# Kernel optimization log

Hardware: AMD Instinct MI355X
Metric: run time of the kernel (lower is better)

The kernel has to match this reference:

```python
import jax, jax.numpy as jnp
import numpy as np

B, S, D = 4, 4096, 1024
STATE = 1024
HID = 4 * D
EPS_NORM = 1e-6           # RMSNorm module eps
EPS_FP32 = 1.1920929e-7   # torch F.rms_norm default eps = finfo(fp32).eps


def rms_norm(x, eps):
    # no learned weight (RMSNorm(dim=-1) has weight=None)
    return x * jax.lax.rsqrt(jnp.mean(jnp.square(x), axis=-1, keepdims=True) + eps)


def setup_inputs() -> dict:
    key = jax.random.key(0)
    ks = jax.random.split(key, 8)
    scale_d = 1.0 / np.sqrt(D)
    scale_s = 1.0 / np.sqrt(STATE)
    scale_h = 1.0 / np.sqrt(HID)
    return {
        "x": jax.random.normal(ks[0], (B, S, D), jnp.float32),
        "x0": jax.random.normal(ks[1], (B, S, D), jnp.float32),
        "Wu": jax.random.normal(ks[2], (STATE, D), jnp.float32) * scale_d,
        "Wg": jax.random.normal(ks[3], (STATE, D), jnp.float32) * scale_d,
        "Wo": jax.random.normal(ks[4], (D, STATE), jnp.float32) * scale_s,
        "Wfc": jax.random.normal(ks[5], (HID, D), jnp.float32) * scale_d,
        "Wproj": jax.random.normal(ks[6], (D, HID), jnp.float32) * scale_h,
        "memory_mix": jnp.ones((D,), jnp.float32),
        "mlp_scale": jnp.ones((D,), jnp.float32),
        "resid_mix": jnp.stack([jnp.ones((D,), jnp.float32), jnp.zeros((D,), jnp.float32)]),
    }


def reference(x, x0, Wu, Wg, Wo, Wfc, Wproj, memory_mix, mlp_scale, resid_mix):
    # residual mix of x and x0
    x = resid_mix[0][None, None, :] * x + resid_mix[1][None, None, :] * x0

    # --- CausalPrefixMemory branch ---
    h = rms_norm(x, EPS_NORM)
    update = jnp.einsum('bsd,kd->bsk', h, Wu)
    gate = jax.nn.sigmoid(jnp.einsum('bsd,kd->bsk', h, Wg))
    memory = jnp.cumsum(gate * update, axis=1)          # [B,S,STATE]
    denom = jnp.arange(1, S + 1, dtype=jnp.float32)[None, :, None]
    m = rms_norm(memory / denom, EPS_FP32)
    mem_out = jnp.einsum('bsk,dk->bsd', m, Wo)
    x = x + memory_mix[None, None, :] * mem_out

    # --- MLP branch: relu^2 ---
    h2 = rms_norm(x, EPS_NORM)
    r = jax.nn.relu(jnp.einsum('bsd,hd->bsh', h2, Wfc))
    mlp_out = jnp.einsum('bsh,dh->bsd', jnp.square(r), Wproj)
    x = x + mlp_scale[None, None, :] * mlp_out
    return x
```

## Files before the change

kernel.cpp:

```cpp
#include <hip/hip_runtime.h>
#include <stdint.h>

typedef unsigned short u16;
typedef __attribute__((ext_vector_type(8))) short s16x8;
typedef __attribute__((ext_vector_type(4))) float f32x4;

__device__ __forceinline__ u16 f2bf(float f) {
  uint32_t u = __float_as_uint(f);
  uint32_t r = (u + 0x7FFFu + ((u >> 16) & 1u)) >> 16;
  return (u16)r;
}

__device__ __forceinline__ void gll16(const void* g, void* lds) {
  __builtin_amdgcn_global_load_lds(
      (const __attribute__((address_space(1))) uint32_t*)g,
      (__attribute__((address_space(3))) uint32_t*)lds, 16, 0, 0);
}

__device__ __forceinline__ void xcd_swz(int& bx, int& by) {
  int gx = gridDim.x;
  int lin = blockIdx.y * gx + blockIdx.x;
  int cpx = (gx * gridDim.y) >> 3;
  int nl = (lin & 7) * cpx + (lin >> 3);
  bx = nl % gx;
  by = nl / gx;
}

__global__ __launch_bounds__(256) void k_f2b(const float* __restrict__ src,
                                             u16* __restrict__ dst, int n) {
  int i = (blockIdx.x * 256 + threadIdx.x) * 4;
  if (i < n) {
    float4 v = *(const float4*)(src + i);
    ushort4 o;
    o.x = f2bf(v.x); o.y = f2bf(v.y); o.z = f2bf(v.z); o.w = f2bf(v.w);
    *(ushort4*)(dst + i) = o;
  }
}

template <bool MIX>
__global__ __launch_bounds__(256) void k_rms(const float* __restrict__ X,
                                             const float* __restrict__ X0,
                                             const float* __restrict__ rmix,
                                             float* __restrict__ XMout,
                                             u16* __restrict__ Hout, float eps) {
  const int row = blockIdx.x, t = threadIdx.x;
  const size_t base = (size_t)row * 1024;
  float4 v;
  if (MIX) {
    float4 a = ((const float4*)(X + base))[t];
    float4 b = ((const float4*)(X0 + base))[t];
    float4 c0 = ((const float4*)rmix)[t];
    float4 c1 = ((const float4*)(rmix + 1024))[t];
    v.x = c0.x * a.x + c1.x * b.x;
    v.y = c0.y * a.y + c1.y * b.y;
    v.z = c0.z * a.z + c1.z * b.z;
    v.w = c0.w * a.w + c1.w * b.w;
  } else {
    v = ((const float4*)(X + base))[t];
  }
  float ss = v.x * v.x + v.y * v.y + v.z * v.z + v.w * v.w;
#pragma unroll
  for (int o = 32; o > 0; o >>= 1) ss += __shfl_xor(ss, o);
  __shared__ float red[4];
  if ((t & 63) == 0) red[t >> 6] = ss;
  __syncthreads();
  float tot = red[0] + red[1] + red[2] + red[3];
  float sc = rsqrtf(tot * (1.0f / 1024.0f) + eps);
  if (MIX) ((float4*)(XMout + base))[t] = v;
  ushort4 hv;
  hv.x = f2bf(v.x * sc); hv.y = f2bf(v.y * sc);
  hv.z = f2bf(v.z * sc); hv.w = f2bf(v.w * sc);
  ((ushort4*)(Hout + base))[t] = hv;
}

__global__ __launch_bounds__(256) void k_rms_mem(const float* __restrict__ Mem,
                                                 u16* __restrict__ Mout) {
  const int row = blockIdx.x, t = threadIdx.x;
  const float inv = 1.0f / (float)((row & 4095) + 1);
  const size_t base = (size_t)row * 1024;
  float4 v = ((const float4*)(Mem + base))[t];
  v.x *= inv; v.y *= inv; v.z *= inv; v.w *= inv;
  float ss = v.x * v.x + v.y * v.y + v.z * v.z + v.w * v.w;
#pragma unroll
  for (int o = 32; o > 0; o >>= 1) ss += __shfl_xor(ss, o);
  __shared__ float red[4];
  if ((t & 63) == 0) red[t >> 6] = ss;
  __syncthreads();
  float tot = red[0] + red[1] + red[2] + red[3];
  float sc = rsqrtf(tot * (1.0f / 1024.0f) + 1.1920929e-7f);
  ushort4 hv;
  hv.x = f2bf(v.x * sc); hv.y = f2bf(v.y * sc);
  hv.z = f2bf(v.z * sc); hv.w = f2bf(v.w * sc);
  ((ushort4*)(Mout + base))[t] = hv;
}

__global__ __launch_bounds__(256) void k_scan1(const float* __restrict__ P,
                                               float* __restrict__ CS) {
  int blk = blockIdx.x;
  int kt = blk & 3, chunk = (blk >> 2) & 15, b = blk >> 6;
  int k = kt * 256 + threadIdx.x;
  const float* p = P + ((size_t)b * 4096 + (size_t)chunk * 256) * 1024 + k;
  float s = 0.f;
#pragma unroll 8
  for (int i = 0; i < 256; ++i) s += p[(size_t)i * 1024];
  CS[((size_t)b * 16 + chunk) * 1024 + k] = s;
}

__global__ __launch_bounds__(256) void k_scan2(float* __restrict__ CS) {
  int idx = blockIdx.x * 256 + threadIdx.x;
  int b = idx >> 10, k = idx & 1023;
  float run = 0.f;
  for (int c = 0; c < 16; ++c) {
    size_t o = ((size_t)b * 16 + c) * 1024 + k;
    float v = CS[o];
    CS[o] = run;
    run += v;
  }
}

__global__ __launch_bounds__(256) void k_scan3(float* __restrict__ P,
                                               const float* __restrict__ CS) {
  int blk = blockIdx.x;
  int kt = blk & 3, chunk = (blk >> 2) & 15, b = blk >> 6;
  int k = kt * 256 + threadIdx.x;
  float run = CS[((size_t)b * 16 + chunk) * 1024 + k];
  float* p = P + ((size_t)b * 4096 + (size_t)chunk * 256) * 1024 + k;
#pragma unroll 8
  for (int i = 0; i < 256; ++i) {
    run += p[(size_t)i * 1024];
    p[(size_t)i * 1024] = run;
  }
}

__global__ __launch_bounds__(256, 2) void gemm_dual(
    const u16* __restrict__ A, const u16* __restrict__ Bu,
    const u16* __restrict__ Bg, float* __restrict__ P, int K) {
  __shared__ __align__(16) u16 As[128 * 64];
  __shared__ __align__(16) u16 Us[64 * 64];
  __shared__ __align__(16) u16 Gs[64 * 64];
  const int t = threadIdx.x;
  const int lane = t & 63, wid = t >> 6;
  int bx, by;
  xcd_swz(bx, by);
  const int m0 = by * 128, n0 = bx * 64;
  const int wm = wid * 32;
  const int l15 = lane & 15, lhi = lane >> 4;

  size_t gA[4], gU[2];
#pragma unroll
  for (int i = 0; i < 4; ++i) {
    int j = i * 256 + t;
    int row = j >> 3;
    int k16 = (j & 7) ^ (row & 7);
    gA[i] = (size_t)(m0 + row) * K + k16 * 8;
  }
#pragma unroll
  for (int i = 0; i < 2; ++i) {
    int j = i * 256 + t;
    int row = j >> 3;
    int k16 = (j & 7) ^ (row & 7);
    gU[i] = (size_t)(n0 + row) * K + k16 * 8;
  }

  f32x4 au[2][4], ag[2][4];
#pragma unroll
  for (int mi = 0; mi < 2; ++mi)
#pragma unroll
    for (int ni = 0; ni < 4; ++ni) { au[mi][ni] = 0.0f; ag[mi][ni] = 0.0f; }

  for (int kb = 0; kb < K; kb += 64) {
#pragma unroll
    for (int i = 0; i < 4; ++i) {
      int j = i * 256 + t;
      gll16(A + gA[i] + kb, &As[j * 8]);
    }
#pragma unroll
    for (int i = 0; i < 2; ++i) {
      int j = i * 256 + t;
      gll16(Bu + gU[i] + kb, &Us[j * 8]);
      gll16(Bg + gU[i] + kb, &Gs[j * 8]);
    }
    __syncthreads();
#pragma unroll
    for (int kc = 0; kc < 2; ++kc) {
      s16x8 af[2], uf[4], gf[4];
#pragma unroll
      for (int mi = 0; mi < 2; ++mi) {
        int row = wm + mi * 16 + l15;
        int k16 = (kc * 4 + lhi) ^ (row & 7);
        af[mi] = *(const s16x8*)&As[row * 64 + k16 * 8];
      }
#pragma unroll
      for (int ni = 0; ni < 4; ++ni) {
        int row = ni * 16 + l15;
        int k16 = (kc * 4 + lhi) ^ (row & 7);
        uf[ni] = *(const s16x8*)&Us[row * 64 + k16 * 8];
        gf[ni] = *(const s16x8*)&Gs[row * 64 + k16 * 8];
      }
#pragma unroll
      for (int mi = 0; mi < 2; ++mi)
#pragma unroll
        for (int ni = 0; ni < 4; ++ni) {
          au[mi][ni] = __builtin_amdgcn_mfma_f32_16x16x32_bf16(
              af[mi], uf[ni], au[mi][ni], 0, 0, 0);
          ag[mi][ni] = __builtin_amdgcn_mfma_f32_16x16x32_bf16(
              af[mi], gf[ni], ag[mi][ni], 0, 0, 0);
        }
    }
    __syncthreads();
  }

#pragma unroll
  for (int mi = 0; mi < 2; ++mi) {
    int r0 = m0 + wm + mi * 16 + lhi * 4;
#pragma unroll
    for (int ni = 0; ni < 4; ++ni) {
      int c = n0 + ni * 16 + l15;
#pragma unroll
      for (int j = 0; j < 4; ++j) {
        float u = au[mi][ni][j], g = ag[mi][ni][j];
        P[(size_t)(r0 + j) * 1024 + c] = u / (1.0f + __expf(-g));
      }
    }
  }
}

template <int EPI>
__global__ __launch_bounds__(256, 2) void gemm_bf16(
    const u16* __restrict__ A, const u16* __restrict__ Bw, void* __restrict__ Cout,
    const float* __restrict__ Cadd, const float* __restrict__ colscale,
    int K, int lda, int ldb, int ldc) {
  __shared__ __align__(16) u16 As[128 * 64];
  __shared__ __align__(16) u16 Bs[128 * 64];
  const int t = threadIdx.x;
  const int lane = t & 63, wid = t >> 6;
  int bx, by;
  xcd_swz(bx, by);
  const int m0 = by * 128, n0 = bx * 128;
  const int wm = (wid >> 1) * 64, wn = (wid & 1) * 64;
  const int l15 = lane & 15, lhi = lane >> 4;

  size_t gA[4], gB[4];
#pragma unroll
  for (int i = 0; i < 4; ++i) {
    int j = i * 256 + t;
    int row = j >> 3;
    int k16 = (j & 7) ^ (row & 7);
    gA[i] = (size_t)(m0 + row) * lda + k16 * 8;
    gB[i] = (size_t)(n0 + row) * ldb + k16 * 8;
  }

  f32x4 acc[4][4];
#pragma unroll
  for (int mi = 0; mi < 4; ++mi)
#pragma unroll
    for (int ni = 0; ni < 4; ++ni) acc[mi][ni] = 0.0f;

  for (int kb = 0; kb < K; kb += 64) {
#pragma unroll
    for (int i = 0; i < 4; ++i) {
      int j = i * 256 + t;
      gll16(A + gA[i] + kb, &As[j * 8]);
      gll16(Bw + gB[i] + kb, &Bs[j * 8]);
    }
    __syncthreads();
#pragma unroll
    for (int kc = 0; kc < 2; ++kc) {
      s16x8 af[4], bfr[4];
#pragma unroll
      for (int mi = 0; mi < 4; ++mi) {
        int row = wm + mi * 16 + l15;
        int k16 = (kc * 4 + lhi) ^ (row & 7);
        af[mi] = *(const s16x8*)&As[row * 64 + k16 * 8];
      }
#pragma unroll
      for (int ni = 0; ni < 4; ++ni) {
        int row = wn + ni * 16 + l15;
        int k16 = (kc * 4 + lhi) ^ (row & 7);
        bfr[ni] = *(const s16x8*)&Bs[row * 64 + k16 * 8];
      }
#pragma unroll
      for (int mi = 0; mi < 4; ++mi)
#pragma unroll
        for (int ni = 0; ni < 4; ++ni)
          acc[mi][ni] = __builtin_amdgcn_mfma_f32_16x16x32_bf16(
              af[mi], bfr[ni], acc[mi][ni], 0, 0, 0);
    }
    __syncthreads();
  }

#pragma unroll
  for (int mi = 0; mi < 4; ++mi) {
    int r0 = m0 + wm + mi * 16 + lhi * 4;
#pragma unroll
    for (int ni = 0; ni < 4; ++ni) {
      int c = n0 + wn + ni * 16 + l15;
      float cs = (EPI == 1) ? colscale[c] : 0.f;
#pragma unroll
      for (int j = 0; j < 4; ++j) {
        size_t idx = (size_t)(r0 + j) * ldc + c;
        float v = acc[mi][ni][j];
        if (EPI == 1) {
          ((float*)Cout)[idx] = Cadd[idx] + cs * v;
        } else {
          float rv = fmaxf(v, 0.f);
          ((u16*)Cout)[idx] = f2bf(rv * rv);
        }
      }
    }
  }
}

extern "C" void kernel_launch(void* const* d_in, const int* in_sizes, int n_in,
                              void* d_out, int out_size, void* d_ws, size_t ws_size,
                              hipStream_t stream) {
  const float* x = (const float*)d_in[0];
  const float* x0 = (const float*)d_in[1];
  const float* Wu = (const float*)d_in[2];
  const float* Wg = (const float*)d_in[3];
  const float* Wo = (const float*)d_in[4];
  const float* Wfc = (const float*)d_in[5];
  const float* Wpj = (const float*)d_in[6];
  const float* mmix = (const float*)d_in[7];
  const float* mscale = (const float*)d_in[8];
  const float* rmix = (const float*)d_in[9];
  float* out = (float*)d_out;

  const int M = 16384;

  char* ws = (char*)d_ws;
  u16* WuB = (u16*)ws;   ws += (size_t)1024 * 1024 * 2;
  u16* WgB = (u16*)ws;   ws += (size_t)1024 * 1024 * 2;
  u16* WoB = (u16*)ws;   ws += (size_t)1024 * 1024 * 2;
  u16* WfcB = (u16*)ws;  ws += (size_t)4096 * 1024 * 2;
  u16* WpjB = (u16*)ws;  ws += (size_t)1024 * 4096 * 2;
  u16* h = (u16*)ws;     ws += (size_t)M * 1024 * 2;
  float* P = (float*)ws; u16* R2 = (u16*)P;
  ws += (size_t)M * 1024 * 4;
  float* CS = (float*)ws; ws += (size_t)4 * 16 * 1024 * 4;
  u16* mB = (u16*)ws;     ws += (size_t)M * 1024 * 2;
  float* xm = out;

  k_f2b<<<1024, 256, 0, stream>>>(Wu, WuB, 1024 * 1024);
  k_f2b<<<1024, 256, 0, stream>>>(Wg, WgB, 1024 * 1024);
  k_f2b<<<1024, 256, 0, stream>>>(Wo, WoB, 1024 * 1024);
  k_f2b<<<4096, 256, 0, stream>>>(Wfc, WfcB, 4096 * 1024);
  k_f2b<<<4096, 256, 0, stream>>>(Wpj, WpjB, 4096 * 1024);

  k_rms<true><<<M, 256, 0, stream>>>(x, x0, rmix, xm, h, 1e-6f);

  gemm_dual<<<dim3(16, 128), 256, 0, stream>>>(h, WuB, WgB, P, 1024);

  k_scan1<<<256, 256, 0, stream>>>(P, CS);
  k_scan2<<<16, 256, 0, stream>>>(CS);
  k_scan3<<<256, 256, 0, stream>>>(P, CS);

  k_rms_mem<<<M, 256, 0, stream>>>(P, mB);

  gemm_bf16<1><<<dim3(8, 128), 256, 0, stream>>>(mB, WoB, xm, xm, mmix,
                                                 1024, 1024, 1024, 1024);
  k_rms<false><<<M, 256, 0, stream>>>(xm, nullptr, nullptr, nullptr, h, 1e-6f);

  for (int c = 0; c < 2; ++c) {
    gemm_bf16<2><<<dim3(16, 128), 256, 0, stream>>>(
        h, WfcB + (size_t)c * 2048 * 1024, R2, nullptr, nullptr,
        1024, 1024, 1024, 2048);
    gemm_bf16<1><<<dim3(8, 128), 256, 0, stream>>>(
        R2, WpjB + (size_t)c * 2048, out, out, mscale,
        2048, 2048, 4096, 1024);
  }
}
```

Before: 551.3 us.

## Replace 128x128 GEMM with 256x256 tile, 4-stage LDS pipelined kernel

Replaces the single-buffered 128x128 bf16 GEMM with a 512-thread 256x256-tile kernel. It uses a 4-slot LDS ring with K-step 32 and prefetches two steps ahead via global_load_lds. Loads are interleaved with the MFMA phases, with barriers, setprio and fine-grained vmcnt waits. The goal is to hide global-load latency and raise data reuse per tile. In exchange it uses fewer, larger blocks (256 blocks for the N=1024 GEMMs), heavier register use, and many barriers per K-step.

```diff
diff --git a/kernel.cpp b/kernel.cpp
--- a/kernel.cpp
+++ b/kernel.cpp
@@ -226,75 +226,103 @@
 }
 
 template <int EPI>
-__global__ __launch_bounds__(256, 2) void gemm_bf16(
-    const u16* __restrict__ A, const u16* __restrict__ Bw, void* __restrict__ Cout,
-    const float* __restrict__ Cadd, const float* __restrict__ colscale,
-    int K, int lda, int ldb, int ldc) {
-  __shared__ __align__(16) u16 As[128 * 64];
-  __shared__ __align__(16) u16 Bs[128 * 64];
+__global__ __launch_bounds__(512, 2) void gemm256(
+    const u16* __restrict__ A, const u16* __restrict__ Bw,
+    void* __restrict__ Cout, const float* __restrict__ Cadd,
+    const float* __restrict__ colscale, int K, int lda, int ldb, int ldc) {
+  __shared__ __align__(16) u16 As[4][8192];
+  __shared__ __align__(16) u16 Bs[4][8192];
   const int t = threadIdx.x;
   const int lane = t & 63, wid = t >> 6;
   int bx, by;
   xcd_swz(bx, by);
-  const int m0 = by * 128, n0 = bx * 128;
-  const int wm = (wid >> 1) * 64, wn = (wid & 1) * 64;
+  const int m0 = by * 256, n0 = bx * 256;
+  const int wr = wid >> 2, wc = wid & 3;
   const int l15 = lane & 15, lhi = lane >> 4;
-
-  size_t gA[4], gB[4];
-#pragma unroll
-  for (int i = 0; i < 4; ++i) {
-    int j = i * 256 + t;
-    int row = j >> 3;
-    int k16 = (j & 7) ^ (row & 7);
-    gA[i] = (size_t)(m0 + row) * lda + k16 * 8;
-    gB[i] = (size_t)(n0 + row) * ldb + k16 * 8;
-  }
-
-  f32x4 acc[4][4];
-#pragma unroll
-  for (int mi = 0; mi < 4; ++mi)
+  const int sphys = (lhi ^ ((l15 >> 1) & 3)) * 8;
+
+  size_t gA[2], gB[2];
+  int soff[2];
+#pragma unroll
+  for (int i = 0; i < 2; ++i) {
+    int idx = i * 512 + t;
+    int row = idx >> 2, sp = idx & 3;
+    int sl = sp ^ ((row >> 1) & 3);
+    gA[i] = (size_t)(m0 + row) * lda + sl * 8;
+    gB[i] = (size_t)(n0 + row) * ldb + sl * 8;
+    soff[i] = row * 32 + sp * 8;
+  }
+
+  f32x4 acc[8][4];
+#pragma unroll
+  for (int mi = 0; mi < 8; ++mi)
 #pragma unroll
     for (int ni = 0; ni < 4; ++ni) acc[mi][ni] = 0.0f;
 
-  for (int kb = 0; kb < K; kb += 64) {
-#pragma unroll
-    for (int i = 0; i < 4; ++i) {
-      int j = i * 256 + t;
-      gll16(A + gA[i] + kb, &As[j * 8]);
-      gll16(Bw + gB[i] + kb, &Bs[j * 8]);
-    }
-    __syncthreads();
-#pragma unroll
-    for (int kc = 0; kc < 2; ++kc) {
-      s16x8 af[4], bfr[4];
-#pragma unroll
-      for (int mi = 0; mi < 4; ++mi) {
-        int row = wm + mi * 16 + l15;
-        int k16 = (kc * 4 + lhi) ^ (row & 7);
-        af[mi] = *(const s16x8*)&As[row * 64 + k16 * 8];
-      }
+  const int nt = K >> 5;
+
+#pragma unroll
+  for (int tt = 0; tt < 2; ++tt) {
+#pragma unroll
+    for (int i = 0; i < 2; ++i) {
+      gll16(A + gA[i] + tt * 32, &As[tt][soff[i]]);
+      gll16(Bw + gB[i] + tt * 32, &Bs[tt][soff[i]]);
+    }
+  }
+  asm volatile("s_waitcnt vmcnt(4)" ::: "memory");
+  __builtin_amdgcn_s_barrier();
+  __builtin_amdgcn_sched_barrier(0);
+
+  for (int kt = 0; kt < nt; ++kt) {
+    const int slot = kt & 3;
+    const u16* as = As[slot];
+    const u16* bs = Bs[slot];
+    const int su = (kt + 2) & 3;
+    const bool st = (kt + 2) < nt;
+    const int kb = (kt + 2) << 5;
+    s16x8 bf[4];
+#pragma unroll
+    for (int q = 0; q < 4; ++q) {
+      if (q == 0) {
+#pragma unroll
+        for (int ni = 0; ni < 4; ++ni)
+          bf[ni] = *(const s16x8*)&bs[(wc * 64 + ni * 16 + l15) * 32 + sphys];
+      }
+      const int r0 = wr * 128 + q * 32 + l15;
+      s16x8 af0 = *(const s16x8*)&as[r0 * 32 + sphys];
+      s16x8 af1 = *(const s16x8*)&as[(r0 + 16) * 32 + sphys];
+      if (st) {
+        if (q == 0) gll16(A + gA[0] + kb, &As[su][soff[0]]);
+        if (q == 1) gll16(A + gA[1] + kb, &As[su][soff[1]]);
+        if (q == 2) gll16(Bw + gB[0] + kb, &Bs[su][soff[0]]);
+        if (q == 3) gll16(Bw + gB[1] + kb, &Bs[su][soff[1]]);
+      }
+      __builtin_amdgcn_s_barrier();
+      __builtin_amdgcn_sched_barrier(0);
+      __builtin_amdgcn_s_setprio(1);
 #pragma unroll
       for (int ni = 0; ni < 4; ++ni) {
-        int row = wn + ni * 16 + l15;
-        int k16 = (kc * 4 + lhi) ^ (row & 7);
-        bfr[ni] = *(const s16x8*)&Bs[row * 64 + k16 * 8];
-      }
-#pragma unroll
-      for (int mi = 0; mi < 4; ++mi)
-#pragma unroll
-        for (int ni = 0; ni < 4; ++ni)
-          acc[mi][ni] = __builtin_amdgcn_mfma_f32_16x16x32_bf16(
-              af[mi], bfr[ni], acc[mi][ni], 0, 0, 0);
-    }
-    __syncthreads();
-  }
-
-#pragma unroll
-  for (int mi = 0; mi < 4; ++mi) {
-    int r0 = m0 + wm + mi * 16 + lhi * 4;
+        acc[2 * q][ni] = __builtin_amdgcn_mfma_f32_16x16x32_bf16(
+            af0, bf[ni], acc[2 * q][ni], 0, 0, 0);
+        acc[2 * q + 1][ni] = __builtin_amdgcn_mfma_f32_16x16x32_bf16(
+            af1, bf[ni], acc[2 * q + 1][ni], 0, 0, 0);
+      }
+      __builtin_amdgcn_s_setprio(0);
+      if (q == 3) {
+        if (st) asm volatile("s_waitcnt vmcnt(4)" ::: "memory");
+        else    asm volatile("s_waitcnt vmcnt(0)" ::: "memory");
+      }
+      __builtin_amdgcn_s_barrier();
+      __builtin_amdgcn_sched_barrier(0);
+    }
+  }
+
+#pragma unroll
+  for (int mi = 0; mi < 8; ++mi) {
+    int r0 = m0 + wr * 128 + mi * 16 + lhi * 4;
 #pragma unroll
     for (int ni = 0; ni < 4; ++ni) {
-      int c = n0 + wn + ni * 16 + l15;
+      int c = n0 + wc * 64 + ni * 16 + l15;
       float cs = (EPI == 1) ? colscale[c] : 0.f;
 #pragma unroll
       for (int j = 0; j < 4; ++j) {
@@ -357,15 +385,15 @@
 
   k_rms_mem<<<M, 256, 0, stream>>>(P, mB);
 
-  gemm_bf16<1><<<dim3(8, 128), 256, 0, stream>>>(mB, WoB, xm, xm, mmix,
-                                                 1024, 1024, 1024, 1024);
+  gemm256<1><<<dim3(4, 64), 512, 0, stream>>>(mB, WoB, xm, xm, mmix,
+                                              1024, 1024, 1024, 1024);
   k_rms<false><<<M, 256, 0, stream>>>(xm, nullptr, nullptr, nullptr, h, 1e-6f);
 
   for (int c = 0; c < 2; ++c) {
-    gemm_bf16<2><<<dim3(16, 128), 256, 0, stream>>>(
+    gemm256<2><<<dim3(8, 64), 512, 0, stream>>>(
         h, WfcB + (size_t)c * 2048 * 1024, R2, nullptr, nullptr,
         1024, 1024, 1024, 2048);
-    gemm_bf16<1><<<dim3(8, 128), 256, 0, stream>>>(
+    gemm256<1><<<dim3(4, 64), 512, 0, stream>>>(
         R2, WpjB + (size_t)c * 2048, out, out, mscale,
         2048, 2048, 4096, 1024);
   }
```

New measurement: 649.7 us. 17.8% more time.

## Vectorize chunked scan with finer chunks and fuse MLP down-projection when workspace allows

Applied to the files above, without the earlier changes.

The prefix-scan kernels now split the sequence into 64 chunks of 64 rows per batch instead of 16 chunks of 256, and each thread handles float4 columns, which gives more blocks and wider loads. The serial carry pass now walks 64 chunk sums instead of 16. When the workspace is large enough, the full 4096-wide relu² activation is materialized so the down-projection runs as one K=4096 GEMM instead of two accumulating passes, avoiding a second read-modify-write of the output. The old split path is kept as a fallback for smaller workspaces.

```diff
diff --git a/kernel.cpp b/kernel.cpp
--- a/kernel.cpp
+++ b/kernel.cpp
@@ -97,21 +97,24 @@
 __global__ __launch_bounds__(256) void k_scan1(const float* __restrict__ P,
                                                float* __restrict__ CS) {
   int blk = blockIdx.x;
-  int kt = blk & 3, chunk = (blk >> 2) & 15, b = blk >> 6;
-  int k = kt * 256 + threadIdx.x;
-  const float* p = P + ((size_t)b * 4096 + (size_t)chunk * 256) * 1024 + k;
-  float s = 0.f;
+  int chunk = blk & 63, b = blk >> 6;
+  const float4* p = (const float4*)(P + ((size_t)b * 4096 + chunk * 64) * 1024)
+                    + threadIdx.x;
+  float4 s = {0.f, 0.f, 0.f, 0.f};
 #pragma unroll 8
-  for (int i = 0; i < 256; ++i) s += p[(size_t)i * 1024];
-  CS[((size_t)b * 16 + chunk) * 1024 + k] = s;
+  for (int i = 0; i < 64; ++i) {
+    float4 v = p[(size_t)i * 256];
+    s.x += v.x; s.y += v.y; s.z += v.z; s.w += v.w;
+  }
+  ((float4*)(CS + ((size_t)b * 64 + chunk) * 1024))[threadIdx.x] = s;
 }
 
 __global__ __launch_bounds__(256) void k_scan2(float* __restrict__ CS) {
   int idx = blockIdx.x * 256 + threadIdx.x;
   int b = idx >> 10, k = idx & 1023;
   float run = 0.f;
-  for (int c = 0; c < 16; ++c) {
-    size_t o = ((size_t)b * 16 + c) * 1024 + k;
+  for (int c = 0; c < 64; ++c) {
+    size_t o = ((size_t)b * 64 + c) * 1024 + k;
     float v = CS[o];
     CS[o] = run;
     run += v;
@@ -121,14 +124,14 @@
 __global__ __launch_bounds__(256) void k_scan3(float* __restrict__ P,
                                                const float* __restrict__ CS) {
   int blk = blockIdx.x;
-  int kt = blk & 3, chunk = (blk >> 2) & 15, b = blk >> 6;
-  int k = kt * 256 + threadIdx.x;
-  float run = CS[((size_t)b * 16 + chunk) * 1024 + k];
-  float* p = P + ((size_t)b * 4096 + (size_t)chunk * 256) * 1024 + k;
+  int chunk = blk & 63, b = blk >> 6;
+  float4 run = ((const float4*)(CS + ((size_t)b * 64 + chunk) * 1024))[threadIdx.x];
+  float4* p = (float4*)(P + ((size_t)b * 4096 + chunk * 64) * 1024) + threadIdx.x;
 #pragma unroll 8
-  for (int i = 0; i < 256; ++i) {
-    run += p[(size_t)i * 1024];
-    p[(size_t)i * 1024] = run;
+  for (int i = 0; i < 64; ++i) {
+    float4 v = p[(size_t)i * 256];
+    run.x += v.x; run.y += v.y; run.z += v.z; run.w += v.w;
+    p[(size_t)i * 256] = run;
   }
 }
 
@@ -327,19 +330,23 @@
   float* out = (float*)d_out;
 
   const int M = 16384;
+  const size_t MiB = 1024 * 1024;
 
   char* ws = (char*)d_ws;
-  u16* WuB = (u16*)ws;   ws += (size_t)1024 * 1024 * 2;
-  u16* WgB = (u16*)ws;   ws += (size_t)1024 * 1024 * 2;
-  u16* WoB = (u16*)ws;   ws += (size_t)1024 * 1024 * 2;
-  u16* WfcB = (u16*)ws;  ws += (size_t)4096 * 1024 * 2;
-  u16* WpjB = (u16*)ws;  ws += (size_t)1024 * 4096 * 2;
-  u16* h = (u16*)ws;     ws += (size_t)M * 1024 * 2;
-  float* P = (float*)ws; u16* R2 = (u16*)P;
-  ws += (size_t)M * 1024 * 4;
-  float* CS = (float*)ws; ws += (size_t)4 * 16 * 1024 * 4;
-  u16* mB = (u16*)ws;     ws += (size_t)M * 1024 * 2;
+  u16* WuB = (u16*)ws;   ws += 2 * MiB;
+  u16* WgB = (u16*)ws;   ws += 2 * MiB;
+  u16* WoB = (u16*)ws;   ws += 2 * MiB;
+  u16* WfcB = (u16*)ws;  ws += 8 * MiB;
+  u16* WpjB = (u16*)ws;  ws += 8 * MiB;
+  u16* h = (u16*)ws;     ws += 32 * MiB;
+  char* pool = ws;
+  float* P = (float*)pool;
+  float* CS = (float*)(pool + 64 * MiB);
+  u16* mB = (u16*)(pool + 65 * MiB);
+  u16* R2 = (u16*)pool;
   float* xm = out;
+
+  const bool fullR2 = ws_size >= 182 * MiB;
 
   k_f2b<<<1024, 256, 0, stream>>>(Wu, WuB, 1024 * 1024);
   k_f2b<<<1024, 256, 0, stream>>>(Wg, WgB, 1024 * 1024);
@@ -361,12 +368,21 @@
                                                  1024, 1024, 1024, 1024);
   k_rms<false><<<M, 256, 0, stream>>>(xm, nullptr, nullptr, nullptr, h, 1e-6f);
 
-  for (int c = 0; c < 2; ++c) {
-    gemm_bf16<2><<<dim3(16, 128), 256, 0, stream>>>(
-        h, WfcB + (size_t)c * 2048 * 1024, R2, nullptr, nullptr,
-        1024, 1024, 1024, 2048);
+  if (fullR2) {
+    for (int c = 0; c < 2; ++c)
+      gemm_bf16<2><<<dim3(16, 128), 256, 0, stream>>>(
+          h, WfcB + (size_t)c * 2048 * 1024, R2 + (size_t)c * 2048, nullptr,
+          nullptr, 1024, 1024, 1024, 4096);
     gemm_bf16<1><<<dim3(8, 128), 256, 0, stream>>>(
-        R2, WpjB + (size_t)c * 2048, out, out, mscale,
-        2048, 2048, 4096, 1024);
-  }
-}
+        R2, WpjB, out, out, mscale, 4096, 4096, 4096, 1024);
+  } else {
+    for (int c = 0; c < 2; ++c) {
+      gemm_bf16<2><<<dim3(16, 128), 256, 0, stream>>>(
+          h, WfcB + (size_t)c * 2048 * 1024, R2, nullptr, nullptr,
+          1024, 1024, 1024, 2048);
+      gemm_bf16<1><<<dim3(8, 128), 256, 0, stream>>>(
+          R2, WpjB + (size_t)c * 2048, out, out, mscale,
+          2048, 2048, 4096, 1024);
+    }
+  }
+}
```

New measurement: 525.8 us. 1.05x faster.
